# Kernel optimization log

Hardware: AMD Instinct MI355X
Metric: run time of the kernel (lower is better)

The kernel has to match this reference:

```python
import jax, jax.numpy as jnp
import numpy as np

DIM = 1024
HIDDEN = 4096
NNZ = 262144
X_SHAPE = (2, 256, DIM)


def setup_inputs() -> dict:
    key = jax.random.key(0)
    ks = jax.random.split(key, 13)
    return {
        "x": jax.random.normal(ks[0], X_SHAPE, dtype=jnp.float32),
        "up_row": jax.random.randint(ks[1], (NNZ,), 0, HIDDEN),
        "up_col": jax.random.randint(ks[2], (NNZ,), 0, DIM),
        "up_val": jax.random.normal(ks[3], (NNZ,), dtype=jnp.float32),
        "up_bias": jax.random.normal(ks[4], (HIDDEN,), dtype=jnp.float32),
        "gate_row": jax.random.randint(ks[5], (NNZ,), 0, HIDDEN),
        "gate_col": jax.random.randint(ks[6], (NNZ,), 0, DIM),
        "gate_val": jax.random.normal(ks[7], (NNZ,), dtype=jnp.float32),
        "gate_bias": jax.random.normal(ks[8], (HIDDEN,), dtype=jnp.float32),
        "down_row": jax.random.randint(ks[9], (NNZ,), 0, DIM),
        "down_col": jax.random.randint(ks[10], (NNZ,), 0, HIDDEN),
        "down_val": jax.random.normal(ks[11], (NNZ,), dtype=jnp.float32),
        "down_bias": jax.random.normal(ks[12], (DIM,), dtype=jnp.float32),
    }


def _sparse_linear(x2d, row, col, val, bias, out_features):
    # x2d: [T, in_features]; COO: row -> out_features, col -> in_features
    weighted = x2d[:, col] * val  # [T, nnz], same expanded form as torch gather*mul
    # scatter_add over rows == segment_sum over the nnz axis
    out = jax.ops.segment_sum(weighted.T, row, num_segments=out_features).T  # [T, out]
    return out + bias


def reference(x, up_row, up_col, up_val, up_bias,
              gate_row, gate_col, gate_val, gate_bias,
              down_row, down_col, down_val, down_bias):
    in_shape = x.shape
    x2d = x.reshape(-1, DIM)  # [T, dim]
    up = _sparse_linear(x2d, up_row, up_col, up_val, up_bias, HIDDEN)
    gate = _sparse_linear(x2d, gate_row, gate_col, gate_val, gate_bias, HIDDEN)
    hidden = jax.nn.silu(up) * gate  # [T, hidden]
    down = _sparse_linear(hidden, down_row, down_col, down_val, down_bias, DIM)
    return (x2d + down).reshape(in_shape)
```

## Files before the change

### kernel.cpp

```cpp
#include <hip/hip_runtime.h>
#include <hip/hip_bf16.h>
#include <stdint.h>


#define DIM_    1024
#define HIDDEN_ 4096
#define NNZ_    262144
#define TTOK_   512
#define PADL_   12

typedef __attribute__((ext_vector_type(8))) short short8;
typedef __attribute__((ext_vector_type(4))) float float4v;

__device__ inline unsigned short f2bf(float f) {
    union { float f; unsigned int u; } c; c.f = f;
    unsigned int u = c.u;
    unsigned int r = u + 0x7fffu + ((u >> 16) & 1u);
    return (unsigned short)(r >> 16);
}

__device__ inline void async16(const unsigned short* g, unsigned short* l) {
    __builtin_amdgcn_global_load_lds(
        (const __attribute__((address_space(1))) unsigned int*)g,
        (__attribute__((address_space(3))) unsigned int*)l, 16, 0, 0);
}

#define XC_ ((TTOK_ * DIM_) / 4)

__global__ __launch_bounds__(256) void bin_prep_kernel(
    const int* __restrict__ ur, const int* __restrict__ uc, const float* __restrict__ uv,
    const int* __restrict__ gr, const int* __restrict__ gc, const float* __restrict__ gv,
    const int* __restrict__ dr, const int* __restrict__ dc, const float* __restrict__ dv,
    const float* __restrict__ x, const float* __restrict__ down_bias,
    unsigned int* __restrict__ bands, int* __restrict__ cnt,
    int* __restrict__ goc, uint2* __restrict__ gof,
    unsigned short* __restrict__ xb, float* __restrict__ out) {
    const int b = blockIdx.x;
    const int t = threadIdx.x;
    if (b >= 768) {
        const unsigned int u0 = (b - 768) * 1024 + t * 4;
        #pragma unroll
        for (int q = 0; q < 4; ++q) {
            const unsigned int id = u0 + q;
            if (id < XC_) {
                float4 v = ((const float4*)x)[id];
                ushort4 o;
                o.x = f2bf(v.x); o.y = f2bf(v.y); o.z = f2bf(v.z); o.w = f2bf(v.w);
                ((ushort4*)xb)[id] = o;
            } else {
                const unsigned int i = id - XC_;
                float4 v = ((const float4*)x)[i];
                const int d = (i * 4) & (DIM_ - 1);
                const float4 bb = *(const float4*)(down_bias + d);
                float4 o;
                o.x = v.x + bb.x; o.y = v.y + bb.y; o.z = v.z + bb.z; o.w = v.w + bb.w;
                ((float4*)out)[i] = o;
            }
        }
        return;
    }
    __shared__ unsigned int stage[256][PADL_];
    __shared__ int lcount[256];
    const int mat = b >> 8;
    const int chunk = b & 255;
    const int*   rs = (mat == 0) ? ur : (mat == 1) ? gr : dr;
    const int*   cs = (mat == 0) ? uc : (mat == 1) ? gc : dc;
    const float* vs = (mat == 0) ? uv : (mat == 1) ? gv : dv;
    const int shift = (mat == 2) ? 2 : 4;
    const int rmask = (mat == 2) ? 3 : 15;
    lcount[t] = 0;
    __syncthreads();

    const int base = chunk * 1024 + t * 4;
    int4   r4 = *(const int4*)(rs + base);
    int4   c4 = *(const int4*)(cs + base);
    float4 v4 = *(const float4*)(vs + base);
    int   rr[4] = {r4.x, r4.y, r4.z, r4.w};
    int   cc[4] = {c4.x, c4.y, c4.z, c4.w};
    float vv[4] = {v4.x, v4.y, v4.z, v4.w};
    #pragma unroll
    for (int j = 0; j < 4; ++j) {
        const int band = rr[j] >> shift;
        const unsigned int e = ((unsigned int)(rr[j] & rmask) << 28)
                             | ((unsigned int)cc[j] << 16)
                             | (unsigned int)f2bf(vv[j]);
        const int pos = atomicAdd(&lcount[band], 1);
        if (pos < PADL_) {
            stage[band][pos] = e;
        } else {
            const int op = atomicAdd(&goc[mat], 1);
            gof[mat * 4096 + op] = make_uint2((unsigned int)band, e);
        }
    }
    __syncthreads();
    unsigned int* seg = bands + ((unsigned int)(mat * 256 + t) * 256 + chunk) * PADL_;
    const uint4* sp = (const uint4*)&stage[t][0];
    *(uint4*)(seg)     = sp[0];
    *(uint4*)(seg + 4) = sp[1];
    *(uint4*)(seg + 8) = sp[2];
    cnt[(mat * 256 + t) * 256 + chunk] = lcount[t];
}

__global__ __launch_bounds__(512) void build_kernel(
    const unsigned int* __restrict__ bands,
    const int* __restrict__ cnt,
    const int* __restrict__ goc, const uint2* __restrict__ gof,
    unsigned short* __restrict__ WUP,
    unsigned short* __restrict__ WGATE,
    unsigned short* __restrict__ WDOWN) {
    __shared__ float acc[8 * 1024];
    __shared__ int lcnt[256];
    const int b = blockIdx.x;
    const int t = threadIdx.x;
    const int mat = b / 512;
    const int rem = b - mat * 512;
    const int band = rem >> 1;
    const int hb = rem & 1;
    unsigned int width, rhalf;
    unsigned short* out;
    if (mat == 0)      { width = 1024; rhalf = 8; out = WUP + (band * 16 + hb * 8) * 1024; }
    else if (mat == 1) { width = 1024; rhalf = 8; out = WGATE + (band * 16 + hb * 8) * 1024; }
    else               { width = 4096; rhalf = 2; out = WDOWN + (band * 4 + hb * 2) * 4096; }
    const unsigned int rbase = hb * rhalf;

    for (int k = 0; k < 4; ++k)
        *(float4*)&acc[(k * 512 + t) * 4] = make_float4(0.f, 0.f, 0.f, 0.f);
    if (t < 256) lcnt[t] = cnt[(mat * 256 + band) * 256 + t];
    __syncthreads();

    const int chunk = t & 255;
    const int half = t >> 8;
    const unsigned int* seg = bands + ((unsigned int)(mat * 256 + band) * 256 + chunk) * PADL_;
    const int c = lcnt[chunk];

    if (half == 0) {
        uint4 q[3];
        const uint4* sp = (const uint4*)seg;
        #pragma unroll
        for (int i = 0; i < 3; ++i) q[i] = sp[i];
        const unsigned int* qq = (const unsigned int*)q;
        #pragma unroll
        for (int j = 0; j < PADL_; ++j) {
            const unsigned int e = qq[j];
            const unsigned int r2 = (e >> 28) - rbase;
            if (j < c && r2 < rhalf)
                atomicAdd(&acc[r2 * width + ((e >> 16) & 0xFFFu)],
                          __uint_as_float(e << 16));
        }
    } else {
        const int oc = goc[mat] < 4096 ? goc[mat] : 4096;
        for (int i = chunk; i < oc; i += 256) {
            uint2 oe = gof[mat * 4096 + i];
            if ((int)oe.x == band) {
                const unsigned int e = oe.y;
                const unsigned int r2 = (e >> 28) - rbase;
                if (r2 < rhalf)
                    atomicAdd(&acc[r2 * width + ((e >> 16) & 0xFFFu)],
                              __uint_as_float(e << 16));
            }
        }
    }
    __syncthreads();

    for (int k = 0; k < 4; ++k) {
        const int cc = (k * 512 + t) * 4;
        ushort4 o;
        o.x = f2bf(acc[cc]);     o.y = f2bf(acc[cc + 1]);
        o.z = f2bf(acc[cc + 2]); o.w = f2bf(acc[cc + 3]);
        *(ushort4*)(out + cc) = o;
    }
}

__global__ __launch_bounds__(256) void gemm_upgate_kernel(
    const unsigned short* __restrict__ xb,
    const unsigned short* __restrict__ wup,
    const unsigned short* __restrict__ wgate,
    const float* __restrict__ up_bias,
    const float* __restrict__ gate_bias,
    unsigned short* __restrict__ hid) {
    __shared__ unsigned short sA[2 * 64 * 32];
    __shared__ unsigned short sBu[2 * 64 * 32];
    __shared__ unsigned short sBg[2 * 64 * 32];
    const int t = threadIdx.x;
    const int n0 = blockIdx.x * 64;
    const int m0 = blockIdx.y * 64;
    const int w = t >> 6, l = t & 63;
    const int wm = (w >> 1) * 32, wn = (w & 1) * 32;
    const int lr = l & 15, lkq = (l >> 4);

    float4v au[2][2], ag[2][2];
    for (int im = 0; im < 2; ++im)
        for (int in = 0; in < 2; ++in) {
            au[im][in] = float4v{0.f, 0.f, 0.f, 0.f};
            ag[im][in] = float4v{0.f, 0.f, 0.f, 0.f};
        }

    const int srow = t >> 2, scol = (t & 3) * 8;
    const unsigned short* gA  = xb    + (m0 + srow) * DIM_ + scol;
    const unsigned short* gBu = wup   + (n0 + srow) * DIM_ + scol;
    const unsigned short* gBg = wgate + (n0 + srow) * DIM_ + scol;

    for (int k0 = 0; k0 < DIM_; k0 += 64) {
        async16(gA + k0,       &sA[t * 8]);
        async16(gA + k0 + 32,  &sA[2048 + t * 8]);
        async16(gBu + k0,      &sBu[t * 8]);
        async16(gBu + k0 + 32, &sBu[2048 + t * 8]);
        async16(gBg + k0,      &sBg[t * 8]);
        async16(gBg + k0 + 32, &sBg[2048 + t * 8]);
        __syncthreads();
        #pragma unroll
        for (int kk = 0; kk < 2; ++kk) {
            const int kb = kk * 2048 + lkq * 8;
            short8 a[2], bu[2], bg[2];
            for (int im = 0; im < 2; ++im)
                a[im] = *(const short8*)&sA[kb + (wm + im * 16 + lr) * 32];
            for (int in = 0; in < 2; ++in) {
                bu[in] = *(const short8*)&sBu[kb + (wn + in * 16 + lr) * 32];
                bg[in] = *(const short8*)&sBg[kb + (wn + in * 16 + lr) * 32];
            }
            for (int im = 0; im < 2; ++im)
                for (int in = 0; in < 2; ++in) {
                    au[im][in] = __builtin_amdgcn_mfma_f32_16x16x32_bf16(
                        a[im], bu[in], au[im][in], 0, 0, 0);
                    ag[im][in] = __builtin_amdgcn_mfma_f32_16x16x32_bf16(
                        a[im], bg[in], ag[im][in], 0, 0, 0);
                }
        }
        __syncthreads();
    }

    for (int im = 0; im < 2; ++im) {
        for (int in = 0; in < 2; ++in) {
            const int n = n0 + wn + in * 16 + lr;
            const float ub = up_bias[n], gb = gate_bias[n];
            for (int r = 0; r < 4; ++r) {
                const int m = m0 + wm + im * 16 + lkq * 4 + r;
                const float u = au[im][in][r] + ub;
                const float g = ag[im][in][r] + gb;
                const float h = (u / (1.f + __expf(-u))) * g;
                hid[m * HIDDEN_ + n] = f2bf(h);
            }
        }
    }
}

__global__ __launch_bounds__(256) void gemm_down_kernel(
    const unsigned short* __restrict__ hid,
    const unsigned short* __restrict__ wdown,
    float* __restrict__ out) {
    __shared__ unsigned short sA[2 * 64 * 32];
    __shared__ unsigned short sB[2 * 64 * 32];
    const int t = threadIdx.x;
    const int n0 = blockIdx.x * 64;
    const int m0 = blockIdx.y * 64;
    const int kb0 = blockIdx.z * 1024;
    const int w = t >> 6, l = t & 63;
    const int wm = (w >> 1) * 32, wn = (w & 1) * 32;
    const int lr = l & 15, lkq = (l >> 4);

    float4v acc[2][2];
    for (int im = 0; im < 2; ++im)
        for (int in = 0; in < 2; ++in)
            acc[im][in] = float4v{0.f, 0.f, 0.f, 0.f};

    const int srow = t >> 2, scol = (t & 3) * 8;
    const unsigned short* gA = hid   + (m0 + srow) * HIDDEN_ + scol;
    const unsigned short* gB = wdown + (n0 + srow) * HIDDEN_ + scol;

    for (int k0 = kb0; k0 < kb0 + 1024; k0 += 64) {
        async16(gA + k0,      &sA[t * 8]);
        async16(gA + k0 + 32, &sA[2048 + t * 8]);
        async16(gB + k0,      &sB[t * 8]);
        async16(gB + k0 + 32, &sB[2048 + t * 8]);
        __syncthreads();
        #pragma unroll
        for (int kk = 0; kk < 2; ++kk) {
            const int kb = kk * 2048 + lkq * 8;
            short8 a[2], b[2];
            for (int im = 0; im < 2; ++im)
                a[im] = *(const short8*)&sA[kb + (wm + im * 16 + lr) * 32];
            for (int in = 0; in < 2; ++in)
                b[in] = *(const short8*)&sB[kb + (wn + in * 16 + lr) * 32];
            for (int im = 0; im < 2; ++im)
                for (int in = 0; in < 2; ++in)
                    acc[im][in] = __builtin_amdgcn_mfma_f32_16x16x32_bf16(
                        a[im], b[in], acc[im][in], 0, 0, 0);
        }
        __syncthreads();
    }

    for (int im = 0; im < 2; ++im) {
        for (int in = 0; in < 2; ++in) {
            const int n = n0 + wn + in * 16 + lr;
            for (int r = 0; r < 4; ++r) {
                const int m = m0 + wm + im * 16 + lkq * 4 + r;
                atomicAdd(out + m * DIM_ + n, acc[im][in][r]);
            }
        }
    }
}

extern "C" void kernel_launch(void* const* d_in, const int* in_sizes, int n_in,
                              void* d_out, int out_size, void* d_ws, size_t ws_size,
                              hipStream_t stream) {
    const float* x         = (const float*)d_in[0];
    const int*   up_row    = (const int*)d_in[1];
    const int*   up_col    = (const int*)d_in[2];
    const float* up_val    = (const float*)d_in[3];
    const float* up_bias   = (const float*)d_in[4];
    const int*   gate_row  = (const int*)d_in[5];
    const int*   gate_col  = (const int*)d_in[6];
    const float* gate_val  = (const float*)d_in[7];
    const float* gate_bias = (const float*)d_in[8];
    const int*   down_row  = (const int*)d_in[9];
    const int*   down_col  = (const int*)d_in[10];
    const float* down_val  = (const float*)d_in[11];
    const float* down_bias = (const float*)d_in[12];
    float* out = (float*)d_out;

    unsigned char* ws = (unsigned char*)d_ws;
    unsigned short* WUP   = (unsigned short*)(ws);
    unsigned short* WGATE = (unsigned short*)(ws + (8u << 20));
    unsigned short* WDOWN = (unsigned short*)(ws + (16u << 20));
    unsigned short* XB    = (unsigned short*)(ws + (24u << 20));
    unsigned short* HID   = (unsigned short*)(ws + (25u << 20));
    unsigned int*   BANDS = (unsigned int*)(ws + (29u << 20));
    int*            CNT   = (int*)(ws + (66u << 20));
    int*            GOC   = (int*)(ws + (67u << 20));
    uint2*          GOF   = (uint2*)(ws + (67u << 20) + 64);

    hipMemsetAsync(GOC, 0, 3 * sizeof(int), stream);

    bin_prep_kernel<<<1024, 256, 0, stream>>>(
        up_row, up_col, up_val, gate_row, gate_col, gate_val,
        down_row, down_col, down_val, x, down_bias, BANDS, CNT, GOC, GOF, XB, out);

    build_kernel<<<1536, 512, 0, stream>>>(BANDS, CNT, GOC, GOF, WUP, WGATE, WDOWN);

    gemm_upgate_kernel<<<dim3(HIDDEN_ / 64, TTOK_ / 64), 256, 0, stream>>>(
        XB, WUP, WGATE, up_bias, gate_bias, HID);

    gemm_down_kernel<<<dim3(DIM_ / 64, TTOK_ / 64, 4), 256, 0, stream>>>(
        HID, WDOWN, out);
}
```

Before: 133.9 us.

## Double-buffer LDS tiles in up/gate and down GEMM kernels

Converts the single-buffered shared-memory K loop in both MFMA GEMM kernels into a two-stage ping-pong pipeline. The async global-to-LDS loads for the next K tile are issued before computing on the current tile, removing one barrier per iteration and overlapping load latency with MFMA work. This doubles LDS use per block, which may reduce occupancy, and it depends on the async loads being correctly waited on before the barrier.

```diff
diff --git a/kernel.cpp b/kernel.cpp
--- a/kernel.cpp
+++ b/kernel.cpp
@@ -171,6 +171,38 @@
     }
 }
 
+#define STAGE_UG(buf, k0)                                      \
+    async16(gA + (k0),       &sA[(buf)][t * 8]);               \
+    async16(gA + (k0) + 32,  &sA[(buf)][2048 + t * 8]);        \
+    async16(gBu + (k0),      &sBu[(buf)][t * 8]);              \
+    async16(gBu + (k0) + 32, &sBu[(buf)][2048 + t * 8]);       \
+    async16(gBg + (k0),      &sBg[(buf)][t * 8]);              \
+    async16(gBg + (k0) + 32, &sBg[(buf)][2048 + t * 8]);
+
+#define COMPUTE_UG(buf)                                                        \
+    _Pragma("unroll")                                                          \
+    for (int kk = 0; kk < 2; ++kk) {                                           \
+        const int kb = kk * 2048 + lkq * 8;                                    \
+        short8 a[2], bu[2], bg[2];                                             \
+        _Pragma("unroll")                                                      \
+        for (int im = 0; im < 2; ++im)                                         \
+            a[im] = *(const short8*)&sA[(buf)][kb + (wm + im * 16 + lr) * 32]; \
+        _Pragma("unroll")                                                      \
+        for (int in = 0; in < 2; ++in) {                                       \
+            bu[in] = *(const short8*)&sBu[(buf)][kb + (wn + in * 16 + lr) * 32]; \
+            bg[in] = *(const short8*)&sBg[(buf)][kb + (wn + in * 16 + lr) * 32]; \
+        }                                                                      \
+        _Pragma("unroll")                                                      \
+        for (int im = 0; im < 2; ++im)                                         \
+            _Pragma("unroll")                                                  \
+            for (int in = 0; in < 2; ++in) {                                   \
+                au[im][in] = __builtin_amdgcn_mfma_f32_16x16x32_bf16(          \
+                    a[im], bu[in], au[im][in], 0, 0, 0);                       \
+                ag[im][in] = __builtin_amdgcn_mfma_f32_16x16x32_bf16(          \
+                    a[im], bg[in], ag[im][in], 0, 0, 0);                       \
+            }                                                                  \
+    }
+
 __global__ __launch_bounds__(256) void gemm_upgate_kernel(
     const unsigned short* __restrict__ xb,
     const unsigned short* __restrict__ wup,
@@ -178,9 +210,9 @@
     const float* __restrict__ up_bias,
     const float* __restrict__ gate_bias,
     unsigned short* __restrict__ hid) {
-    __shared__ unsigned short sA[2 * 64 * 32];
-    __shared__ unsigned short sBu[2 * 64 * 32];
-    __shared__ unsigned short sBg[2 * 64 * 32];
+    __shared__ unsigned short sA[2][2 * 64 * 32];
+    __shared__ unsigned short sBu[2][2 * 64 * 32];
+    __shared__ unsigned short sBg[2][2 * 64 * 32];
     const int t = threadIdx.x;
     const int n0 = blockIdx.x * 64;
     const int m0 = blockIdx.y * 64;
@@ -200,34 +232,17 @@
     const unsigned short* gBu = wup   + (n0 + srow) * DIM_ + scol;
     const unsigned short* gBg = wgate + (n0 + srow) * DIM_ + scol;
 
-    for (int k0 = 0; k0 < DIM_; k0 += 64) {
-        async16(gA + k0,       &sA[t * 8]);
-        async16(gA + k0 + 32,  &sA[2048 + t * 8]);
-        async16(gBu + k0,      &sBu[t * 8]);
-        async16(gBu + k0 + 32, &sBu[2048 + t * 8]);
-        async16(gBg + k0,      &sBg[t * 8]);
-        async16(gBg + k0 + 32, &sBg[2048 + t * 8]);
+    STAGE_UG(0, 0);
+    __syncthreads();
+    int cur = 0;
+    for (int k0 = 64; k0 < DIM_; k0 += 64) {
+        const int nxt = cur ^ 1;
+        STAGE_UG(nxt, k0);
+        COMPUTE_UG(cur);
         __syncthreads();
-        #pragma unroll
-        for (int kk = 0; kk < 2; ++kk) {
-            const int kb = kk * 2048 + lkq * 8;
-            short8 a[2], bu[2], bg[2];
-            for (int im = 0; im < 2; ++im)
-                a[im] = *(const short8*)&sA[kb + (wm + im * 16 + lr) * 32];
-            for (int in = 0; in < 2; ++in) {
-                bu[in] = *(const short8*)&sBu[kb + (wn + in * 16 + lr) * 32];
-                bg[in] = *(const short8*)&sBg[kb + (wn + in * 16 + lr) * 32];
-            }
-            for (int im = 0; im < 2; ++im)
-                for (int in = 0; in < 2; ++in) {
-                    au[im][in] = __builtin_amdgcn_mfma_f32_16x16x32_bf16(
-                        a[im], bu[in], au[im][in], 0, 0, 0);
-                    ag[im][in] = __builtin_amdgcn_mfma_f32_16x16x32_bf16(
-                        a[im], bg[in], ag[im][in], 0, 0, 0);
-                }
-        }
-        __syncthreads();
-    }
+        cur = nxt;
+    }
+    COMPUTE_UG(cur);
 
     for (int im = 0; im < 2; ++im) {
         for (int in = 0; in < 2; ++in) {
@@ -244,12 +259,37 @@
     }
 }
 
+#define STAGE_DN(buf, k0)                                      \
+    async16(gA + (k0),      &sA[(buf)][t * 8]);                \
+    async16(gA + (k0) + 32, &sA[(buf)][2048 + t * 8]);         \
+    async16(gB + (k0),      &sB[(buf)][t * 8]);                \
+    async16(gB + (k0) + 32, &sB[(buf)][2048 + t * 8]);
+
+#define COMPUTE_DN(buf)                                                        \
+    _Pragma("unroll")                                                          \
+    for (int kk = 0; kk < 2; ++kk) {                                           \
+        const int kb = kk * 2048 + lkq * 8;                                    \
+        short8 a[2], b2[2];                                                    \
+        _Pragma("unroll")                                                      \
+        for (int im = 0; im < 2; ++im)                                         \
+            a[im] = *(const short8*)&sA[(buf)][kb + (wm + im * 16 + lr) * 32]; \
+        _Pragma("unroll")                                                      \
+        for (int in = 0; in < 2; ++in)                                         \
+            b2[in] = *(const short8*)&sB[(buf)][kb + (wn + in * 16 + lr) * 32]; \
+        _Pragma("unroll")                                                      \
+        for (int im = 0; im < 2; ++im)                                         \
+            _Pragma("unroll")                                                  \
+            for (int in = 0; in < 2; ++in)                                     \
+                acc[im][in] = __builtin_amdgcn_mfma_f32_16x16x32_bf16(         \
+                    a[im], b2[in], acc[im][in], 0, 0, 0);                      \
+    }
+
 __global__ __launch_bounds__(256) void gemm_down_kernel(
     const unsigned short* __restrict__ hid,
     const unsigned short* __restrict__ wdown,
     float* __restrict__ out) {
-    __shared__ unsigned short sA[2 * 64 * 32];
-    __shared__ unsigned short sB[2 * 64 * 32];
+    __shared__ unsigned short sA[2][2 * 64 * 32];
+    __shared__ unsigned short sB[2][2 * 64 * 32];
     const int t = threadIdx.x;
     const int n0 = blockIdx.x * 64;
     const int m0 = blockIdx.y * 64;
@@ -267,27 +307,17 @@
     const unsigned short* gA = hid   + (m0 + srow) * HIDDEN_ + scol;
     const unsigned short* gB = wdown + (n0 + srow) * HIDDEN_ + scol;
 
-    for (int k0 = kb0; k0 < kb0 + 1024; k0 += 64) {
-        async16(gA + k0,      &sA[t * 8]);
-        async16(gA + k0 + 32, &sA[2048 + t * 8]);
-        async16(gB + k0,      &sB[t * 8]);
-        async16(gB + k0 + 32, &sB[2048 + t * 8]);
+    STAGE_DN(0, kb0);
+    __syncthreads();
+    int cur = 0;
+    for (int k0 = kb0 + 64; k0 < kb0 + 1024; k0 += 64) {
+        const int nxt = cur ^ 1;
+        STAGE_DN(nxt, k0);
+        COMPUTE_DN(cur);
         __syncthreads();
-        #pragma unroll
-        for (int kk = 0; kk < 2; ++kk) {
-            const int kb = kk * 2048 + lkq * 8;
-            short8 a[2], b[2];
-            for (int im = 0; im < 2; ++im)
-                a[im] = *(const short8*)&sA[kb + (wm + im * 16 + lr) * 32];
-            for (int in = 0; in < 2; ++in)
-                b[in] = *(const short8*)&sB[kb + (wn + in * 16 + lr) * 32];
-            for (int im = 0; im < 2; ++im)
-                for (int in = 0; in < 2; ++in)
-                    acc[im][in] = __builtin_amdgcn_mfma_f32_16x16x32_bf16(
-                        a[im], b[in], acc[im][in], 0, 0, 0);
-        }
-        __syncthreads();
-    }
+        cur = nxt;
+    }
+    COMPUTE_DN(cur);
 
     for (int im = 0; im < 2; ++im) {
         for (int in = 0; in < 2; ++in) {
```

Measured after the change: 138.0 us. 1.03x slower.
